# Kernel tuning notes

Measured on AMD Instinct MI355X. Metric: run time of the kernel, lower is better.

## Reference

```python
import jax, jax.numpy as jnp
import numpy as np

SIZES = [1024, 4096, 4096, 4096, 1024]  # layer widths
BATCH = 8192


def setup_inputs() -> dict:
    key = jax.random.key(0)
    keys = jax.random.split(key, 1 + 6 * 4)
    inp = {"x": jax.random.normal(keys[0], (BATCH, SIZES[0]), dtype=jnp.float32)}
    k = 1
    for j, (din, dout) in enumerate(zip(SIZES[:-1], SIZES[1:])):
        scale = 1.0 / np.sqrt(din)
        inp[f"mw{j}"] = jax.random.normal(keys[k], (dout, din), dtype=jnp.float32) * scale; k += 1
        inp[f"sw{j}"] = jax.random.normal(keys[k], (dout, din), dtype=jnp.float32) * scale; k += 1
        inp[f"zw{j}"] = jax.random.normal(keys[k], (dout, din), dtype=jnp.float32); k += 1
        inp[f"mb{j}"] = jax.random.normal(keys[k], (dout,), dtype=jnp.float32) * scale; k += 1
        inp[f"sb{j}"] = jax.random.normal(keys[k], (dout,), dtype=jnp.float32) * scale; k += 1
        inp[f"zb{j}"] = jax.random.normal(keys[k], (dout,), dtype=jnp.float32); k += 1
    return inp


def reference(x,
              mw0, sw0, zw0, mb0, sb0, zb0,
              mw1, sw1, zw1, mb1, sb1, zb1,
              mw2, sw2, zw2, mb2, sb2, zb2,
              mw3, sw3, zw3, mb3, sb3, zb3):
    layers = [
        (mw0, sw0, zw0, mb0, sb0, zb0),
        (mw1, sw1, zw1, mb1, sb1, zb1),
        (mw2, sw2, zw2, mb2, sb2, zb2),
        (mw3, sw3, zw3, mb3, sb3, zb3),
    ]
    n = len(layers)
    h = x
    for j, (mw, sw, zw, mb, sb, zb) in enumerate(layers):
        # rho(sigma) = log(1 + exp(sigma)) == softplus; reparameterized weight sample
        A = mw + jax.nn.softplus(sw) * zw          # [out, in]
        b = mb + jax.nn.softplus(sb) * zb          # [out]
        h = h @ A.T + b                             # [B, out]
        if j < n - 1:                               # activation between Linear layers
            h = jnp.tanh(h)
    return h
```

## Files before the change

### kernel.cpp

```cpp
#include <hip/hip_runtime.h>
#include <cstdint>
#include <cstddef>

typedef _Float16 f16;
typedef _Float16 f16x8 __attribute__((ext_vector_type(8)));
typedef float    fx4   __attribute__((ext_vector_type(4)));


__device__ __forceinline__ float softplus_f(float x) {
    return (x > 20.0f) ? x : log1pf(expf(x));
}

__global__ void prep_w_kernel(const float* __restrict__ mw, const float* __restrict__ sw,
                              const float* __restrict__ zw, f16* __restrict__ hi,
                              f16* __restrict__ lo, int n) {
    int i = (blockIdx.x * blockDim.x + threadIdx.x) * 4;
    if (i >= n) return;
    float4 m4 = *(const float4*)(mw + i);
    float4 s4 = *(const float4*)(sw + i);
    float4 z4 = *(const float4*)(zw + i);
    float a[4];
    a[0] = m4.x + softplus_f(s4.x) * z4.x;
    a[1] = m4.y + softplus_f(s4.y) * z4.y;
    a[2] = m4.z + softplus_f(s4.z) * z4.z;
    a[3] = m4.w + softplus_f(s4.w) * z4.w;
    f16 h4[4], l4[4];
#pragma unroll
    for (int j = 0; j < 4; ++j) {
        h4[j] = (f16)a[j];
        l4[j] = (f16)(a[j] - (float)h4[j]);
    }
    *(short4*)(hi + i) = *(short4*)h4;
    if (lo) *(short4*)(lo + i) = *(short4*)l4;
}

__global__ void prep_b_kernel(const float* __restrict__ mb, const float* __restrict__ sb,
                              const float* __restrict__ zb, float* __restrict__ b, int n) {
    int i = blockIdx.x * blockDim.x + threadIdx.x;
    if (i < n) b[i] = mb[i] + softplus_f(sb[i]) * zb[i];
}

__global__ void split_x_kernel(const float* __restrict__ x, f16* __restrict__ hi,
                               f16* __restrict__ lo, int n) {
    int i = (blockIdx.x * blockDim.x + threadIdx.x) * 4;
    if (i >= n) return;
    float4 v = *(const float4*)(x + i);
    float a[4] = {v.x, v.y, v.z, v.w};
    f16 h4[4], l4[4];
#pragma unroll
    for (int j = 0; j < 4; ++j) {
        h4[j] = (f16)a[j];
        l4[j] = (f16)(a[j] - (float)h4[j]);
    }
    *(short4*)(hi + i) = *(short4*)h4;
    *(short4*)(lo + i) = *(short4*)l4;
}

__device__ __forceinline__ void cp16(const f16* g, f16* l) {
    __builtin_amdgcn_global_load_lds((__attribute__((address_space(1))) void*)g,
                                     (__attribute__((address_space(3))) void*)l,
                                     16, 0, 0);
}


#define PHASE_SYNC(V)                                          \
    asm volatile("s_waitcnt vmcnt(" V ")" ::: "memory");       \
    __builtin_amdgcn_s_barrier();                              \
    __builtin_amdgcn_sched_barrier(0);

template <int OUT>
__global__ __launch_bounds__(512, 1) void gemm256_split3_kernel(
    const f16* __restrict__ Hhi, const f16* __restrict__ Hlo,
    const f16* __restrict__ Whi, const f16* __restrict__ Wlo,
    const float* __restrict__ bias,
    f16* __restrict__ Ohi, f16* __restrict__ Olo,
    int M, int N, int K)
{
    __shared__ __align__(16) f16 lds[2][4][8192];

    const int tid  = threadIdx.x;
    const int lane = tid & 63;
    const int wave = tid >> 6;
    const int wm   = wave >> 2;
    const int wn   = wave & 3;
    const int col  = lane & 15;
    const int quad = lane >> 4;

    const int nwg = gridDim.x * gridDim.y;
    const int bid = blockIdx.y * gridDim.x + blockIdx.x;
    const int swz = (bid & 7) * (nwg >> 3) + (bid >> 3);
    const int bx  = swz % gridDim.x;
    const int by  = swz / gridDim.x;
    const int mBase = by * 256;
    const int nBase = bx * 256;

    const int    srow = tid >> 2;
    const int    kc   = (tid & 3) ^ ((tid >> 3) & 3);
    const size_t aoff0 = (size_t)(mBase + srow) * K + kc * 8;
    const size_t aoff1 = aoff0 + (size_t)128 * K;
    const size_t boff0 = (size_t)(nBase + srow) * K + kc * 8;
    const size_t boff1 = boff0 + (size_t)128 * K;

    const int NK = K >> 5;

    auto stage = [&](int j) {
        f16* d = &lds[j & 1][0][0];
        const int k0 = j * 32;
        cp16(Hhi + aoff0 + k0, d + tid * 8);
        cp16(Hhi + aoff1 + k0, d + tid * 8 + 4096);
        cp16(Whi + boff0 + k0, d + 8192  + tid * 8);
        cp16(Whi + boff1 + k0, d + 8192  + tid * 8 + 4096);
        cp16(Wlo + boff0 + k0, d + 16384 + tid * 8);
        cp16(Wlo + boff1 + k0, d + 16384 + tid * 8 + 4096);
        cp16(Hlo + aoff0 + k0, d + 24576 + tid * 8);
        cp16(Hlo + aoff1 + k0, d + 24576 + tid * 8 + 4096);
    };

    float bias_v[4];
#pragma unroll
    for (int nf = 0; nf < 4; ++nf)
        bias_v[nf] = bias[nBase + wn * 64 + nf * 16 + col];

    stage(0);

    fx4 acc[8][4];
#pragma unroll
    for (int i = 0; i < 8; ++i)
#pragma unroll
        for (int j = 0; j < 4; ++j)
            acc[i][j] = (fx4){0.f, 0.f, 0.f, 0.f};

    const int lane_off = col * 32 + ((quad ^ ((col >> 1) & 3)) << 3);
    const int aRow = wm * 128;
    const int bRow = wn * 64;

    f16x8 ah[8], bh[4], bl[4], al[8];

#define KB_BODY(V0, V1, V2, DO_STAGE, KB)                                          \
    {                                                                              \
        PHASE_SYNC(V0)                                                             \
        if (DO_STAGE) stage((KB) + 1);                                             \
        const f16* P = &lds[(KB) & 1][0][0];                                       \
        _Pragma("unroll")                                                          \
        for (int nf = 0; nf < 4; ++nf)                                             \
            bh[nf] = *(const f16x8*)&P[8192 + (bRow + nf * 16) * 32 + lane_off];   \
        _Pragma("unroll")                                                          \
        for (int mf = 0; mf < 8; ++mf)                                             \
            ah[mf] = *(const f16x8*)&P[(aRow + mf * 16) * 32 + lane_off];          \
        __builtin_amdgcn_s_setprio(1);                                             \
        _Pragma("unroll")                                                          \
        for (int mf = 0; mf < 8; ++mf)                                             \
            _Pragma("unroll")                                                      \
            for (int nf = 0; nf < 4; ++nf)                                         \
                acc[mf][nf] = __builtin_amdgcn_mfma_f32_16x16x32_f16(              \
                    ah[mf], bh[nf], acc[mf][nf], 0, 0, 0);                         \
        __builtin_amdgcn_s_setprio(0);                                             \
        PHASE_SYNC(V1)                                                             \
        _Pragma("unroll")                                                          \
        for (int nf = 0; nf < 4; ++nf)                                             \
            bl[nf] = *(const f16x8*)&P[16384 + (bRow + nf * 16) * 32 + lane_off];  \
        __builtin_amdgcn_s_setprio(1);                                             \
        _Pragma("unroll")                                                          \
        for (int mf = 0; mf < 8; ++mf)                                             \
            _Pragma("unroll")                                                      \
            for (int nf = 0; nf < 4; ++nf)                                         \
                acc[mf][nf] = __builtin_amdgcn_mfma_f32_16x16x32_f16(              \
                    ah[mf], bl[nf], acc[mf][nf], 0, 0, 0);                         \
        __builtin_amdgcn_s_setprio(0);                                             \
        PHASE_SYNC(V2)                                                             \
        _Pragma("unroll")                                                          \
        for (int mf = 0; mf < 8; ++mf)                                             \
            al[mf] = *(const f16x8*)&P[24576 + (aRow + mf * 16) * 32 + lane_off];  \
        __builtin_amdgcn_s_setprio(1);                                             \
        _Pragma("unroll")                                                          \
        for (int mf = 0; mf < 8; ++mf)                                             \
            _Pragma("unroll")                                                      \
            for (int nf = 0; nf < 4; ++nf)                                         \
                acc[mf][nf] = __builtin_amdgcn_mfma_f32_16x16x32_f16(              \
                    al[mf], bh[nf], acc[mf][nf], 0, 0, 0);                         \
        __builtin_amdgcn_s_setprio(0);                                             \
    }

    for (int kb = 0; kb + 1 < NK; ++kb)
        KB_BODY("4", "10", "8", true, kb)
    KB_BODY("4", "2", "0", false, NK - 1)

#undef KB_BODY

#pragma unroll
    for (int mf = 0; mf < 8; ++mf)
#pragma unroll
        for (int nf = 0; nf < 4; ++nf) {
            const int n = nBase + wn * 64 + nf * 16 + col;
#pragma unroll
            for (int r = 0; r < 4; ++r) {
                const int m = mBase + wm * 128 + mf * 16 + quad * 4 + r;
                float v = acc[mf][nf][r] + bias_v[nf];
                size_t idx = (size_t)m * N + n;
                float t = tanhf(v);
                f16 thi = (f16)t;
                Ohi[idx] = thi;
                if constexpr (OUT == 1) Olo[idx] = (f16)(t - (float)thi);
            }
        }
}


template <int SPLIT, int OUT>
__global__ __launch_bounds__(512, 2) void gemm256_kernel(
    const f16* __restrict__ Hhi, const f16* __restrict__ Hlo,
    const f16* __restrict__ Whi, const f16* __restrict__ Wlo,
    const float* __restrict__ bias,
    f16* __restrict__ Ohi, f16* __restrict__ Olo, float* __restrict__ Of,
    int M, int N, int K)
{
    __shared__ __align__(16) f16 lds[4][2][8192];

    const int tid  = threadIdx.x;
    const int lane = tid & 63;
    const int wave = tid >> 6;
    const int wm   = wave >> 2;
    const int wn   = wave & 3;
    const int col  = lane & 15;
    const int quad = lane >> 4;

    const int nwg = gridDim.x * gridDim.y;
    const int bid = blockIdx.y * gridDim.x + blockIdx.x;
    const int swz = (bid & 7) * (nwg >> 3) + (bid >> 3);
    const int bx  = swz % gridDim.x;
    const int by  = swz / gridDim.x;
    const int mBase = by * 256;
    const int nBase = bx * 256;

    const int    srow = tid >> 2;
    const int    kc   = (tid & 3) ^ ((tid >> 3) & 3);
    const size_t aoff0 = (size_t)(mBase + srow) * K + kc * 8;
    const size_t aoff1 = aoff0 + (size_t)128 * K;
    const size_t boff0 = (size_t)(nBase + srow) * K + kc * 8;
    const size_t boff1 = boff0 + (size_t)128 * K;

    const int NT = K >> 5;

    auto stageA = [&](int j) {
        f16* d = &lds[j & 3][0][0];
        cp16(Hhi + aoff0 + j * 32, d + tid * 8);
        cp16(Hhi + aoff1 + j * 32, d + tid * 8 + 4096);
    };
    auto stageB = [&](int j) {
        f16* d = &lds[j & 3][1][0];
        cp16(Whi + boff0 + j * 32, d + tid * 8);
        cp16(Whi + boff1 + j * 32, d + tid * 8 + 4096);
    };

    stageA(0); stageB(0); stageA(1); stageB(1); stageA(2); stageB(2);

    float bias_v[4];
#pragma unroll
    for (int nf = 0; nf < 4; ++nf)
        bias_v[nf] = bias[nBase + wn * 64 + nf * 16 + col];

    fx4 acc[8][4];
#pragma unroll
    for (int i = 0; i < 8; ++i)
#pragma unroll
        for (int j = 0; j < 4; ++j)
            acc[i][j] = (fx4){0.f, 0.f, 0.f, 0.f};

    const int lane_off = col * 32 + ((quad ^ ((col >> 1) & 3)) << 3);
    const int aRow = wm * 128;
    const int bRow = wn * 64;

    for (int s = 0; s < NT; ++s) {
        if (s < NT - 2)       asm volatile("s_waitcnt vmcnt(8)" ::: "memory");
        else if (s == NT - 2) asm volatile("s_waitcnt vmcnt(4)" ::: "memory");
        else                  asm volatile("s_waitcnt vmcnt(0)" ::: "memory");
        __builtin_amdgcn_s_barrier();
        __builtin_amdgcn_sched_barrier(0);

        const f16* As = &lds[s & 3][0][0];
        const f16* Bs = &lds[s & 3][1][0];

        f16x8 bfr[4], afr[4];
#pragma unroll
        for (int nf = 0; nf < 4; ++nf)
            bfr[nf] = *(const f16x8*)&Bs[(bRow + nf * 16) * 32 + lane_off];
#pragma unroll
        for (int mf = 0; mf < 4; ++mf)
            afr[mf] = *(const f16x8*)&As[(aRow + mf * 16) * 32 + lane_off];
        if (s + 3 < NT) stageA(s + 3);

        __builtin_amdgcn_s_setprio(1);
#pragma unroll
        for (int mf = 0; mf < 4; ++mf)
#pragma unroll
            for (int nf = 0; nf < 4; ++nf)
                acc[mf][nf] = __builtin_amdgcn_mfma_f32_16x16x32_f16(afr[mf], bfr[nf], acc[mf][nf], 0, 0, 0);
        __builtin_amdgcn_s_setprio(0);

#pragma unroll
        for (int mf = 0; mf < 4; ++mf)
            afr[mf] = *(const f16x8*)&As[(aRow + 64 + mf * 16) * 32 + lane_off];
        if (s + 3 < NT) stageB(s + 3);

        __builtin_amdgcn_s_setprio(1);
#pragma unroll
        for (int mf = 0; mf < 4; ++mf)
#pragma unroll
            for (int nf = 0; nf < 4; ++nf)
                acc[4 + mf][nf] = __builtin_amdgcn_mfma_f32_16x16x32_f16(afr[mf], bfr[nf], acc[4 + mf][nf], 0, 0, 0);
        __builtin_amdgcn_s_setprio(0);
    }

#pragma unroll
    for (int mf = 0; mf < 8; ++mf)
#pragma unroll
        for (int nf = 0; nf < 4; ++nf) {
            const int n = nBase + wn * 64 + nf * 16 + col;
#pragma unroll
            for (int r = 0; r < 4; ++r) {
                const int m = mBase + wm * 128 + mf * 16 + quad * 4 + r;
                float v = acc[mf][nf][r] + bias_v[nf];
                size_t idx = (size_t)m * N + n;
                if constexpr (OUT == 2) {
                    Of[idx] = v;
                } else {
                    float t = tanhf(v);
                    f16 thi = (f16)t;
                    Ohi[idx] = thi;
                    if constexpr (OUT == 1) Olo[idx] = (f16)(t - (float)thi);
                }
            }
        }
}


template <int SPLIT, int OUT>
__global__ __launch_bounds__(256) void gemm_kernel(
    const f16* __restrict__ Hhi, const f16* __restrict__ Hlo,
    const f16* __restrict__ Whi, const f16* __restrict__ Wlo,
    const float* __restrict__ bias,
    f16* __restrict__ Ohi, f16* __restrict__ Olo, float* __restrict__ Of,
    int M, int N, int K)
{
    constexpr int LDSN = 128 * 32;
    __shared__ __align__(16) f16 Hs[(SPLIT ? 2 : 1) * LDSN];
    __shared__ __align__(16) f16 Ws[(SPLIT ? 2 : 1) * LDSN];

    const int tid  = threadIdx.x;
    const int lane = tid & 63;
    const int wave = tid >> 6;
    const int wm   = wave >> 1;
    const int wn   = wave & 1;
    const int col  = lane & 15;
    const int quad = lane >> 4;
    const int mBase = blockIdx.y * 128;
    const int nBase = blockIdx.x * 128;

    float bias_v[4];
#pragma unroll
    for (int nt = 0; nt < 4; ++nt)
        bias_v[nt] = bias[nBase + wn * 64 + nt * 16 + col];

    fx4 acc[4][4];
#pragma unroll
    for (int i = 0; i < 4; ++i)
#pragma unroll
        for (int j = 0; j < 4; ++j)
            acc[i][j] = (fx4){0.f, 0.f, 0.f, 0.f};

    const int c0 = wave * 128 + lane;

    for (int k0 = 0; k0 < K; k0 += 32) {
        __syncthreads();
#pragma unroll
        for (int i = 0; i < 2; ++i) {
            int c  = c0 + i * 64;
            int r  = c >> 2;
            int cc = c & 3;
            size_t gh = (size_t)(mBase + r) * K + k0 + cc * 8;
            size_t gw = (size_t)(nBase + r) * K + k0 + cc * 8;
            cp16(Hhi + gh, &Hs[c * 8]);
            cp16(Whi + gw, &Ws[c * 8]);
            if constexpr (SPLIT) {
                cp16(Hlo + gh, &Hs[LDSN + c * 8]);
                cp16(Wlo + gw, &Ws[LDSN + c * 8]);
            }
        }
        __syncthreads();

        f16x8 bh[4], bl[4];
#pragma unroll
        for (int nt = 0; nt < 4; ++nt) {
            int off = (wn * 64 + nt * 16 + col) * 32 + quad * 8;
            bh[nt] = *(const f16x8*)&Ws[off];
            if constexpr (SPLIT) bl[nt] = *(const f16x8*)&Ws[LDSN + off];
        }
#pragma unroll
        for (int mt = 0; mt < 4; ++mt) {
            int off = (wm * 64 + mt * 16 + col) * 32 + quad * 8;
            f16x8 ah = *(const f16x8*)&Hs[off];
            f16x8 al;
            if constexpr (SPLIT) al = *(const f16x8*)&Hs[LDSN + off];
#pragma unroll
            for (int nt = 0; nt < 4; ++nt) {
                acc[mt][nt] = __builtin_amdgcn_mfma_f32_16x16x32_f16(ah, bh[nt], acc[mt][nt], 0, 0, 0);
                if constexpr (SPLIT) {
                    acc[mt][nt] = __builtin_amdgcn_mfma_f32_16x16x32_f16(ah, bl[nt], acc[mt][nt], 0, 0, 0);
                    acc[mt][nt] = __builtin_amdgcn_mfma_f32_16x16x32_f16(al, bh[nt], acc[mt][nt], 0, 0, 0);
                }
            }
        }
    }

#pragma unroll
    for (int mt = 0; mt < 4; ++mt) {
#pragma unroll
        for (int nt = 0; nt < 4; ++nt) {
            int n = nBase + wn * 64 + nt * 16 + col;
#pragma unroll
            for (int r = 0; r < 4; ++r) {
                int m = mBase + wm * 64 + mt * 16 + quad * 4 + r;
                float v = acc[mt][nt][r] + bias_v[nt];
                size_t idx = (size_t)m * N + n;
                if constexpr (OUT == 2) {
                    Of[idx] = v;
                } else {
                    float t = tanhf(v);
                    f16 thi = (f16)t;
                    Ohi[idx] = thi;
                    if constexpr (OUT == 1) Olo[idx] = (f16)(t - (float)thi);
                }
            }
        }
    }
}


extern "C" void kernel_launch(void* const* d_in, const int* in_sizes, int n_in,
                              void* d_out, int out_size, void* d_ws, size_t ws_size,
                              hipStream_t stream) {
    const int BATCH = 8192;
    const int sizes[5] = {1024, 4096, 4096, 4096, 1024};

    char* ws = (char*)d_ws;
    f16*   x_hi  = (f16*)(ws + 0);
    f16*   x_lo  = (f16*)(ws + 16777216ULL);
    f16*   A0_hi = (f16*)(ws + 33554432ULL);
    f16*   A0_lo = (f16*)(ws + 41943040ULL);
    f16*   A_hi  = (f16*)(ws + 0);
    f16*   A_lo  = (f16*)(ws + 33554432ULL);
    f16*   H0_hi = (f16*)(ws + 67108864ULL);
    f16*   H0_lo = (f16*)(ws + 134217728ULL);
    f16*   H1_hi = (f16*)(ws + 201326592ULL);
    f16*   H2_hi = (f16*)(ws + 67108864ULL);
    float* bb    = (float*)(ws + 268435456ULL);

    const float* x = (const float*)d_in[0];
    const float* p[4][6];
    for (int j = 0; j < 4; ++j)
        for (int t = 0; t < 6; ++t)
            p[j][t] = (const float*)d_in[1 + j * 6 + t];

    {
        int n = BATCH * sizes[0];
        split_x_kernel<<<n / 4 / 256, 256, 0, stream>>>(x, x_hi, x_lo, n);
    }

    {
        int n = sizes[1] * sizes[0];
        prep_w_kernel<<<n / 4 / 256, 256, 0, stream>>>(p[0][0], p[0][1], p[0][2], A0_hi, A0_lo, n);
        prep_b_kernel<<<(sizes[1] + 255) / 256, 256, 0, stream>>>(p[0][3], p[0][4], p[0][5], bb, sizes[1]);
        dim3 grid(sizes[1] / 256, BATCH / 256);
        gemm256_split3_kernel<1><<<grid, 512, 0, stream>>>(
            x_hi, x_lo, A0_hi, A0_lo, bb, H0_hi, H0_lo, BATCH, sizes[1], sizes[0]);
    }

    {
        int n = sizes[2] * sizes[1];
        prep_w_kernel<<<n / 4 / 256, 256, 0, stream>>>(p[1][0], p[1][1], p[1][2], A_hi, A_lo, n);
        prep_b_kernel<<<(sizes[2] + 255) / 256, 256, 0, stream>>>(p[1][3], p[1][4], p[1][5], bb, sizes[2]);
        dim3 grid(sizes[2] / 256, BATCH / 256);
        gemm256_split3_kernel<0><<<grid, 512, 0, stream>>>(
            H0_hi, H0_lo, A_hi, A_lo, bb, H1_hi, nullptr, BATCH, sizes[2], sizes[1]);
    }

    {
        int n = sizes[3] * sizes[2];
        prep_w_kernel<<<n / 4 / 256, 256, 0, stream>>>(p[2][0], p[2][1], p[2][2], A_hi, nullptr, n);
        prep_b_kernel<<<(sizes[3] + 255) / 256, 256, 0, stream>>>(p[2][3], p[2][4], p[2][5], bb, sizes[3]);
        dim3 grid(sizes[3] / 256, BATCH / 256);
        gemm256_kernel<0, 0><<<grid, 512, 0, stream>>>(
            H1_hi, nullptr, A_hi, nullptr, bb, H2_hi, nullptr, nullptr, BATCH, sizes[3], sizes[2]);
    }

    {
        int n = sizes[4] * sizes[3];
        prep_w_kernel<<<n / 4 / 256, 256, 0, stream>>>(p[3][0], p[3][1], p[3][2], A_hi, nullptr, n);
        prep_b_kernel<<<(sizes[4] + 255) / 256, 256, 0, stream>>>(p[3][3], p[3][4], p[3][5], bb, sizes[4]);
        dim3 grid(sizes[4] / 128, BATCH / 128);
        gemm_kernel<0, 2><<<grid, 256, 0, stream>>>(
            H2_hi, nullptr, A_hi, nullptr, bb, nullptr, nullptr, (float*)d_out, BATCH, sizes[4], sizes[3]);
    }
}
```

Measured before the change: 1.725 ms.

## Simplify GEMM pipelines to double-buffered single-wait loops

The split3 kernel drops its three-phase partial-wait schedule. It now waits for all loads with vmcnt(0), issues the next stage, loads every fragment, then runs the three MFMA groups. The non-split 256 kernel goes from a 4-deep A/B-staged pipeline to a 2-stage double buffer with full waits, and uses half the LDS. This cuts scheduling complexity and LDS footprint, but it risks exposing memory latency because prefetch depth is reduced and fine-grained overlap is lost.

```diff
diff --git a/kernel.cpp b/kernel.cpp
--- a/kernel.cpp
+++ b/kernel.cpp
@@ -63,11 +63,6 @@
 }
 
 
-#define PHASE_SYNC(V)                                          \
-    asm volatile("s_waitcnt vmcnt(" V ")" ::: "memory");       \
-    __builtin_amdgcn_s_barrier();                              \
-    __builtin_amdgcn_sched_barrier(0);
-
 template <int OUT>
 __global__ __launch_bounds__(512, 1) void gemm256_split3_kernel(
     const f16* __restrict__ Hhi, const f16* __restrict__ Hlo,
@@ -134,58 +129,52 @@
     const int aRow = wm * 128;
     const int bRow = wn * 64;
 
-    f16x8 ah[8], bh[4], bl[4], al[8];
-
-#define KB_BODY(V0, V1, V2, DO_STAGE, KB)                                          \
-    {                                                                              \
-        PHASE_SYNC(V0)                                                             \
-        if (DO_STAGE) stage((KB) + 1);                                             \
-        const f16* P = &lds[(KB) & 1][0][0];                                       \
-        _Pragma("unroll")                                                          \
-        for (int nf = 0; nf < 4; ++nf)                                             \
-            bh[nf] = *(const f16x8*)&P[8192 + (bRow + nf * 16) * 32 + lane_off];   \
-        _Pragma("unroll")                                                          \
-        for (int mf = 0; mf < 8; ++mf)                                             \
-            ah[mf] = *(const f16x8*)&P[(aRow + mf * 16) * 32 + lane_off];          \
-        __builtin_amdgcn_s_setprio(1);                                             \
-        _Pragma("unroll")                                                          \
-        for (int mf = 0; mf < 8; ++mf)                                             \
-            _Pragma("unroll")                                                      \
-            for (int nf = 0; nf < 4; ++nf)                                         \
-                acc[mf][nf] = __builtin_amdgcn_mfma_f32_16x16x32_f16(              \
-                    ah[mf], bh[nf], acc[mf][nf], 0, 0, 0);                         \
-        __builtin_amdgcn_s_setprio(0);                                             \
-        PHASE_SYNC(V1)                                                             \
-        _Pragma("unroll")                                                          \
-        for (int nf = 0; nf < 4; ++nf)                                             \
-            bl[nf] = *(const f16x8*)&P[16384 + (bRow + nf * 16) * 32 + lane_off];  \
-        __builtin_amdgcn_s_setprio(1);                                             \
-        _Pragma("unroll")                                                          \
-        for (int mf = 0; mf < 8; ++mf)                                             \
-            _Pragma("unroll")                                                      \
-            for (int nf = 0; nf < 4; ++nf)                                         \
-                acc[mf][nf] = __builtin_amdgcn_mfma_f32_16x16x32_f16(              \
-                    ah[mf], bl[nf], acc[mf][nf], 0, 0, 0);                         \
-        __builtin_amdgcn_s_setprio(0);                                             \
-        PHASE_SYNC(V2)                                                             \
-        _Pragma("unroll")                                                          \
-        for (int mf = 0; mf < 8; ++mf)                                             \
-            al[mf] = *(const f16x8*)&P[24576 + (aRow + mf * 16) * 32 + lane_off];  \
-        __builtin_amdgcn_s_setprio(1);                                             \
-        _Pragma("unroll")                                                          \
-        for (int mf = 0; mf < 8; ++mf)                                             \
-            _Pragma("unroll")                                                      \
-            for (int nf = 0; nf < 4; ++nf)                                         \
-                acc[mf][nf] = __builtin_amdgcn_mfma_f32_16x16x32_f16(              \
-                    al[mf], bh[nf], acc[mf][nf], 0, 0, 0);                         \
-        __builtin_amdgcn_s_setprio(0);                                             \
-    }
-
-    for (int kb = 0; kb + 1 < NK; ++kb)
-        KB_BODY("4", "10", "8", true, kb)
-    KB_BODY("4", "2", "0", false, NK - 1)
-
-#undef KB_BODY
+    for (int kb = 0; kb < NK; ++kb) {
+        asm volatile("s_waitcnt vmcnt(0)" ::: "memory");
+        __builtin_amdgcn_s_barrier();
+        __builtin_amdgcn_sched_barrier(0);
+
+        if (kb + 1 < NK) stage(kb + 1);
+
+        const f16* P = &lds[kb & 1][0][0];
+        f16x8 ah[8], bh[4], bl[4], al[8];
+#pragma unroll
+        for (int nf = 0; nf < 4; ++nf)
+            bh[nf] = *(const f16x8*)&P[8192 + (bRow + nf * 16) * 32 + lane_off];
+#pragma unroll
+        for (int mf = 0; mf < 8; ++mf)
+            ah[mf] = *(const f16x8*)&P[(aRow + mf * 16) * 32 + lane_off];
+#pragma unroll
+        for (int nf = 0; nf < 4; ++nf)
+            bl[nf] = *(const f16x8*)&P[16384 + (bRow + nf * 16) * 32 + lane_off];
+#pragma unroll
+        for (int mf = 0; mf < 8; ++mf)
+            al[mf] = *(const f16x8*)&P[24576 + (aRow + mf * 16) * 32 + lane_off];
+
+        __builtin_amdgcn_s_setprio(1);
+#pragma unroll
+        for (int mf = 0; mf < 8; ++mf)
+#pragma unroll
+            for (int nf = 0; nf < 4; ++nf)
+                acc[mf][nf] = __builtin_amdgcn_mfma_f32_16x16x32_f16(ah[mf], bh[nf], acc[mf][nf], 0, 0, 0);
+        __builtin_amdgcn_s_setprio(0);
+
+        __builtin_amdgcn_s_setprio(1);
+#pragma unroll
+        for (int mf = 0; mf < 8; ++mf)
+#pragma unroll
+            for (int nf = 0; nf < 4; ++nf)
+                acc[mf][nf] = __builtin_amdgcn_mfma_f32_16x16x32_f16(ah[mf], bl[nf], acc[mf][nf], 0, 0, 0);
+        __builtin_amdgcn_s_setprio(0);
+
+        __builtin_amdgcn_s_setprio(1);
+#pragma unroll
+        for (int mf = 0; mf < 8; ++mf)
+#pragma unroll
+            for (int nf = 0; nf < 4; ++nf)
+                acc[mf][nf] = __builtin_amdgcn_mfma_f32_16x16x32_f16(al[mf], bh[nf], acc[mf][nf], 0, 0, 0);
+        __builtin_amdgcn_s_setprio(0);
+    }
 
 #pragma unroll
     for (int mf = 0; mf < 8; ++mf)
@@ -206,15 +195,14 @@
 }
 
 
-template <int SPLIT, int OUT>
-__global__ __launch_bounds__(512, 2) void gemm256_kernel(
-    const f16* __restrict__ Hhi, const f16* __restrict__ Hlo,
-    const f16* __restrict__ Whi, const f16* __restrict__ Wlo,
+template <int OUT>
+__global__ __launch_bounds__(512, 2) void gemm256_ns_kernel(
+    const f16* __restrict__ Hhi, const f16* __restrict__ Whi,
     const float* __restrict__ bias,
-    f16* __restrict__ Ohi, f16* __restrict__ Olo, float* __restrict__ Of,
+    f16* __restrict__ Ohi, float* __restrict__ Of,
     int M, int N, int K)
 {
-    __shared__ __align__(16) f16 lds[4][2][8192];
+    __shared__ __align__(16) f16 lds[2][2][8192];
 
     const int tid  = threadIdx.x;
     const int lane = tid & 63;
@@ -239,25 +227,23 @@
     const size_t boff0 = (size_t)(nBase + srow) * K + kc * 8;
     const size_t boff1 = boff0 + (size_t)128 * K;
 
-    const int NT = K >> 5;
-
-    auto stageA = [&](int j) {
-        f16* d = &lds[j & 3][0][0];
-        cp16(Hhi + aoff0 + j * 32, d + tid * 8);
-        cp16(Hhi + aoff1 + j * 32, d + tid * 8 + 4096);
+    const int NK = K >> 5;
+
+    auto stage = [&](int j) {
+        f16* d = &lds[j & 1][0][0];
+        const int k0 = j * 32;
+        cp16(Hhi + aoff0 + k0, d + tid * 8);
+        cp16(Hhi + aoff1 + k0, d + tid * 8 + 4096);
+        cp16(Whi + boff0 + k0, d + 8192 + tid * 8);
+        cp16(Whi + boff1 + k0, d + 8192 + tid * 8 + 4096);
     };
-    auto stageB = [&](int j) {
-        f16* d = &lds[j & 3][1][0];
-        cp16(Whi + boff0 + j * 32, d + tid * 8);
-        cp16(Whi + boff1 + j * 32, d + tid * 8 + 4096);
-    };
-
-    stageA(0); stageB(0); stageA(1); stageB(1); stageA(2); stageB(2);
 
     float bias_v[4];
 #pragma unroll
     for (int nf = 0; nf < 4; ++nf)
         bias_v[nf] = bias[nBase + wn * 64 + nf * 16 + col];
+
+    stage(0);
 
     fx4 acc[8][4];
 #pragma unroll
@@ -270,44 +256,28 @@
     const int aRow = wm * 128;
     const int bRow = wn * 64;
 
-    for (int s = 0; s < NT; ++s) {
-        if (s < NT - 2)       asm volatile("s_waitcnt vmcnt(8)" ::: "memory");
-        else if (s == NT - 2) asm volatile("s_waitcnt vmcnt(4)" ::: "memory");
-        else                  asm volatile("s_waitcnt vmcnt(0)" ::: "memory");
+    for (int kb = 0; kb < NK; ++kb) {
+        asm volatile("s_waitcnt vmcnt(0)" ::: "memory");
         __builtin_amdgcn_s_barrier();
         __builtin_amdgcn_sched_barrier(0);
 
-        const f16* As = &lds[s & 3][0][0];
-        const f16* Bs = &lds[s & 3][1][0];
-
-        f16x8 bfr[4], afr[4];
+        if (kb + 1 < NK) stage(kb + 1);
+
+        const f16* P = &lds[kb & 1][0][0];
+        f16x8 ah[8], bh[4];
 #pragma unroll
         for (int nf = 0; nf < 4; ++nf)
-            bfr[nf] = *(const f16x8*)&Bs[(bRow + nf * 16) * 32 + lane_off];
-#pragma unroll
-        for (int mf = 0; mf < 4; ++mf)
-            afr[mf] = *(const f16x8*)&As[(aRow + mf * 16) * 32 + lane_off];
-        if (s + 3 < NT) stageA(s + 3);
+            bh[nf] = *(const f16x8*)&P[8192 + (bRow + nf * 16) * 32 + lane_off];
+#pragma unroll
+        for (int mf = 0; mf < 8; ++mf)
+            ah[mf] = *(const f16x8*)&P[(aRow + mf * 16) * 32 + lane_off];
 
         __builtin_amdgcn_s_setprio(1);
 #pragma unroll
-        for (int mf = 0; mf < 4; ++mf)
+        for (int mf = 0; mf < 8; ++mf)
 #pragma unroll
             for (int nf = 0; nf < 4; ++nf)
-                acc[mf][nf] = __builtin_amdgcn_mfma_f32_16x16x32_f16(afr[mf], bfr[nf], acc[mf][nf], 0, 0, 0);
-        __builtin_amdgcn_s_setprio(0);
-
-#pragma unroll
-        for (int mf = 0; mf < 4; ++mf)
-            afr[mf] = *(const f16x8*)&As[(aRow + 64 + mf * 16) * 32 + lane_off];
-        if (s + 3 < NT) stageB(s + 3);
-
-        __builtin_amdgcn_s_setprio(1);
-#pragma unroll
-        for (int mf = 0; mf < 4; ++mf)
-#pragma unroll
-            for (int nf = 0; nf < 4; ++nf)
-                acc[4 + mf][nf] = __builtin_amdgcn_mfma_f32_16x16x32_f16(afr[mf], bfr[nf], acc[4 + mf][nf], 0, 0, 0);
+                acc[mf][nf] = __builtin_amdgcn_mfma_f32_16x16x32_f16(ah[mf], bh[nf], acc[mf][nf], 0, 0, 0);
         __builtin_amdgcn_s_setprio(0);
     }
 
@@ -325,9 +295,7 @@
                     Of[idx] = v;
                 } else {
                     float t = tanhf(v);
-                    f16 thi = (f16)t;
-                    Ohi[idx] = thi;
-                    if constexpr (OUT == 1) Olo[idx] = (f16)(t - (float)thi);
+                    Ohi[idx] = (f16)t;
                 }
             }
         }
@@ -489,8 +457,8 @@
         prep_w_kernel<<<n / 4 / 256, 256, 0, stream>>>(p[2][0], p[2][1], p[2][2], A_hi, nullptr, n);
         prep_b_kernel<<<(sizes[3] + 255) / 256, 256, 0, stream>>>(p[2][3], p[2][4], p[2][5], bb, sizes[3]);
         dim3 grid(sizes[3] / 256, BATCH / 256);
-        gemm256_kernel<0, 0><<<grid, 512, 0, stream>>>(
-            H1_hi, nullptr, A_hi, nullptr, bb, H2_hi, nullptr, nullptr, BATCH, sizes[3], sizes[2]);
+        gemm256_ns_kernel<0><<<grid, 512, 0, stream>>>(
+            H1_hi, A_hi, bb, H2_hi, nullptr, BATCH, sizes[3], sizes[2]);
     }
 
     {
```

After: 1.710 ms. No clear change (-0.8%).
